# Performance work log

Measured on AMD Instinct MI355X. Metric: run time of the kernel, lower is better.

## Reference

```python
import jax, jax.numpy as jnp
import numpy as np
from jax import lax

B, W, RSS, NLED, LED_F, HID = 8192, 512, 12, 16, 8, 64


def setup_inputs() -> dict:
    key = jax.random.key(0)
    ks = jax.random.split(key, 20)
    s = 0.05
    return {
        "rss_chunk": jax.random.normal(ks[0], (B, W, RSS), jnp.float32),
        "anchor_pos": jax.random.normal(ks[1], (B, 3), jnp.float32),
        "led_feats": jax.random.normal(ks[2], (NLED, LED_F), jnp.float32),
        "led_positions": jax.random.normal(ks[3], (NLED, 3), jnp.float32),
        "freq_mask": jax.random.randint(ks[4], (RSS, NLED), 0, 2, jnp.int32),
        # temporal_conv params (torch Conv1d weight layout [out, in, k])
        "conv1_w": jax.random.normal(ks[5], (32, RSS, 3), jnp.float32) * s,
        "conv1_b": jax.random.normal(ks[6], (32,), jnp.float32) * s,
        "conv2_w": jax.random.normal(ks[7], (64, 32, 3), jnp.float32) * s,
        "conv2_b": jax.random.normal(ks[8], (64,), jnp.float32) * s,
        # projections (torch Linear weight layout [out, in])
        "q_w": jax.random.normal(ks[9], (64, W + 3), jnp.float32) * s,
        "q_b": jax.random.normal(ks[10], (64,), jnp.float32) * s,
        "k_w": jax.random.normal(ks[11], (64, LED_F + 3), jnp.float32) * s,
        "k_b": jax.random.normal(ks[12], (64,), jnp.float32) * s,
        "red_w": jax.random.normal(ks[13], (64, RSS * LED_F), jnp.float32) * s,
        "red_b": jax.random.normal(ks[14], (64,), jnp.float32) * s,
        "fus_w": jax.random.normal(ks[15], (HID, 64 + 64), jnp.float32) * s,
        "fus_b": jax.random.normal(ks[16], (HID,), jnp.float32) * s,
    }


def _conv1d(x, w, b, stride):
    # x: [B, C_in, L], w: [C_out, C_in, k], padding 1
    y = lax.conv_general_dilated(x, w, (stride,), [(1, 1)],
                                 dimension_numbers=("NCH", "OIH", "NCH"))
    return y + b[None, :, None]


def reference(rss_chunk, anchor_pos, led_feats, led_positions, freq_mask,
              conv1_w, conv1_b, conv2_w, conv2_b,
              q_w, q_b, k_w, k_b, red_w, red_b, fus_w, fus_b):
    Bc = rss_chunk.shape[0]
    x = jnp.swapaxes(rss_chunk, 1, 2)                       # [B, 12, W]

    # temporal conv branch -> [B, 64]
    h = jax.nn.relu(_conv1d(x, conv1_w, conv1_b, 1))        # [B, 32, W]
    h = jax.nn.relu(_conv1d(h, conv2_w, conv2_b, 2))        # [B, 64, W//2]
    t_feat = h.mean(axis=-1)                                # AdaptiveAvgPool1d(1)

    # queries: [B, 12, W+3] -> [B, 12, 64]
    pos_rep = jnp.broadcast_to(anchor_pos[:, None, :], (Bc, RSS, 3))
    query_in = jnp.concatenate([x, pos_rep], axis=-1)
    queries = query_in @ q_w.T + q_b

    # keys: [N, 11] -> [N, 64] (shared across batch)
    key_in = jnp.concatenate([led_feats, led_positions], axis=-1)
    keys = key_in @ k_w.T + k_b

    scores = jnp.einsum("brd,nd->brn", queries, keys)       # [B, 12, N]
    dist_sq = jnp.sum((anchor_pos[:, None, :] - led_positions[None, :, :]) ** 2, -1)
    dist_bias = 0.5 * jnp.log(1.0 / (dist_sq + 1e-8))       # [B, N]
    scores = scores + dist_bias[:, None, :]
    scores = jnp.where(freq_mask[None] == 0, jnp.finfo(scores.dtype).min, scores)

    attn = jax.nn.softmax(scores, axis=-1)                  # [B, 12, N]
    s_agg = jnp.einsum("brn,nf->brf", attn, led_feats)      # [B, 12, 8]
    s_feat = jax.nn.relu(s_agg.reshape(Bc, -1) @ red_w.T + red_b)  # [B, 64]

    combined = jnp.concatenate([t_feat, s_feat], axis=-1)   # [B, 128]
    return combined @ fus_w.T + fus_b                       # [B, hidden]
```

## Files before the change

kernel.cpp:

```cpp
#include <hip/hip_runtime.h>
#include <float.h>
#include <math.h>

typedef __bf16 bf16;
typedef __attribute__((ext_vector_type(8))) __bf16 bf16x8;
typedef __attribute__((ext_vector_type(4))) float f32x4;
typedef long long i64;

#define MK 544

#define WS_MG   0
#define WS_CVEC 17408
#define WS_W1F  17472
#define WS_W2F  19520

__device__ __forceinline__ f32x4 mfma16(bf16x8 a, bf16x8 b, f32x4 c) {
  return __builtin_amdgcn_mfma_f32_16x16x32_bf16(a, b, c, 0, 0, 0);
}
__device__ __forceinline__ f32x4 mfma8(i64 a, i64 b, f32x4 c) {
  return __builtin_amdgcn_mfma_f32_16x16x32_fp8_fp8(a, b, c, 0, 0, 0);
}

__global__ __launch_bounds__(256) void acek_pre(
    const float* __restrict__ led_feats, const float* __restrict__ led_pos,
    const float* __restrict__ q_w, const float* __restrict__ q_b,
    const float* __restrict__ k_w, const float* __restrict__ k_b,
    const float* __restrict__ c1w, const float* __restrict__ c2w,
    char* __restrict__ ws) {
  bf16* Mg = (bf16*)(ws + WS_MG);
  float* cvec = (float*)(ws + WS_CVEC);
  i64* W1F = (i64*)(ws + WS_W1F);
  i64* W2F = (i64*)(ws + WS_W2F);
  const int t = threadIdx.x;

  if (blockIdx.x == 34) {
    {
      int ot = t >> 7, s = (t >> 6) & 1, lane = t & 63;
      int g = lane >> 4, a15 = lane & 15;
      float v[8];
#pragma unroll
      for (int j = 0; j < 8; ++j) {
        int k1 = s * 32 + g * 8 + j;
        int dk = k1 >> 4, ic = k1 & 15;
        v[j] = (ic < 12 && dk < 3) ? 16.f * c1w[(ot * 16 + a15) * 36 + ic * 3 + dk] : 0.f;
      }
      int lo = __builtin_amdgcn_cvt_pk_fp8_f32(v[0], v[1], 0, false);
      lo = __builtin_amdgcn_cvt_pk_fp8_f32(v[2], v[3], lo, true);
      int hi = __builtin_amdgcn_cvt_pk_fp8_f32(v[4], v[5], 0, false);
      hi = __builtin_amdgcn_cvt_pk_fp8_f32(v[6], v[7], hi, true);
      W1F[t] = ((i64)(unsigned)lo) | (((i64)hi) << 32);
    }
    for (int r = 0; r < 3; ++r) {
      int fi = t + r * 256;
      int o = fi / 192, rem = fi - o * 192;
      int s = rem >> 6, lane = rem & 63;
      int g = lane >> 4, a15 = lane & 15;
      float v[8];
#pragma unroll
      for (int j = 0; j < 8; ++j)
        v[j] = 16.f * c2w[(o * 16 + a15) * 96 + (g * 8 + j) * 3 + s];
      int lo = __builtin_amdgcn_cvt_pk_fp8_f32(v[0], v[1], 0, false);
      lo = __builtin_amdgcn_cvt_pk_fp8_f32(v[2], v[3], lo, true);
      int hi = __builtin_amdgcn_cvt_pk_fp8_f32(v[4], v[5], 0, false);
      hi = __builtin_amdgcn_cvt_pk_fp8_f32(v[6], v[7], hi, true);
      W2F[fi] = ((i64)(unsigned)lo) | (((i64)hi) << 32);
    }
    return;
  }

  __shared__ float keys[16 * 64];
  for (int idx = t; idx < 16 * 64; idx += 256) {
    int n = idx >> 6, d = idx & 63;
    float acc = k_b[d];
#pragma unroll
    for (int j = 0; j < 8; ++j) acc += k_w[d * 11 + j] * led_feats[n * 8 + j];
#pragma unroll
    for (int j = 0; j < 3; ++j) acc += k_w[d * 11 + 8 + j] * led_pos[n * 3 + j];
    keys[idx] = acc;
  }
  __syncthreads();
  int e = blockIdx.x * 256 + t;
  if (e < 16 * MK) {
    int n = e / MK, k = e - n * MK;
    float v = 0.f;
    if (k < 515) {
#pragma unroll 4
      for (int d = 0; d < 64; ++d) v += q_w[d * 515 + k] * keys[n * 64 + d];
    }
    Mg[e] = (bf16)v;
  }
  if (blockIdx.x == 0 && t < 16) {
    float acc = 0.f;
    for (int d = 0; d < 64; ++d) acc += q_b[d] * keys[t * 64 + d];
    cvec[t] = acc;
  }
}

__global__ __launch_bounds__(256, 4) void acek_main(
    const float* __restrict__ rss, const float* __restrict__ anchor,
    const float* __restrict__ ledf, const float* __restrict__ ledp,
    const int* __restrict__ fmask,
    const float* __restrict__ c1b, const float* __restrict__ c2b,
    const float* __restrict__ rw, const float* __restrict__ rb,
    const float* __restrict__ fw, const float* __restrict__ fb,
    const bf16* __restrict__ Mg, const float* __restrict__ cvec,
    const i64* __restrict__ W1F, const i64* __restrict__ W2F,
    float* __restrict__ out) {

  __shared__ __align__(16) unsigned char xw8[515 * 16];
  __shared__ __align__(16) unsigned char h1[513 * 32];
  __shared__ __align__(16) float parts[1024];
  __shared__ __align__(16) float sagg[96];
  __shared__ __align__(16) float bias_lds[16];
  __shared__ __align__(16) float tfp[256];
  __shared__ __align__(16) float comb[128];

  const int tid = threadIdx.x;
  const int lane = tid & 63;
  const int wv = tid >> 6;
  const int a15 = lane & 15;
  const int g = lane >> 4;
  const int b = blockIdx.x;
  char* xwb = (char*)xw8;
  char* h1b = (char*)h1;

  i64 w1f[2][2];
#pragma unroll
  for (int ot = 0; ot < 2; ++ot)
#pragma unroll
    for (int s = 0; s < 2; ++s) w1f[ot][s] = W1F[(ot * 2 + s) * 64 + lane];
  i64 w2f[4][3];
#pragma unroll
  for (int o = 0; o < 4; ++o)
#pragma unroll
    for (int s = 0; s < 3; ++s) w2f[o][s] = W2F[(o * 3 + s) * 64 + lane];
  f32x4 b1v[2], b2s[4];
#pragma unroll
  for (int ot = 0; ot < 2; ++ot) b1v[ot] = *(const f32x4*)&c1b[ot * 16 + g * 4];
#pragma unroll
  for (int o = 0; o < 4; ++o) {
    f32x4 tmp = *(const f32x4*)&c2b[o * 16 + g * 4];
    b2s[o] = tmp * 16.f;
  }

  if (wv == 0 && lane < 4) *(int*)(xwb + lane * 4) = 0;
  if (wv == 3 && lane < 8)
    *(int*)(xwb + (513 + (lane >> 2)) * 16 + (lane & 3) * 4) = 0;
  if (wv == 0 && lane >= 4 && lane < 8)
    *(i64*)(h1b + (lane - 4) * 8) = 0;
#pragma unroll
  for (int i = 0; i < 3; ++i) {
    int k = lane + 64 * i;
    int r = wv * 128 - 1 + k;
    if (k < 132 && r >= 0 && r <= 514) *(int*)(xwb + r * 16 + 12) = 0;
  }
  if (tid < 16) {
    float dx = anchor[(size_t)b * 3 + 0] - ledp[tid * 3 + 0];
    float dy = anchor[(size_t)b * 3 + 1] - ledp[tid * 3 + 1];
    float dz = anchor[(size_t)b * 3 + 2] - ledp[tid * 3 + 2];
    bias_lds[tid] = cvec[tid] - 0.5f * __logf(dx * dx + dy * dy + dz * dz + 1e-8f);
  }

  const float* xb = rss + (size_t)b * 6144;
  const f32x4* xb4 = (const f32x4*)xb;
  auto stage_px = [&](int w, int hc, f32x4 v) {
    int pk = __builtin_amdgcn_cvt_pk_fp8_f32(16.f * v[0], 16.f * v[1], 0, false);
    pk = __builtin_amdgcn_cvt_pk_fp8_f32(16.f * v[2], 16.f * v[3], pk, true);
    *(int*)(xwb + (w + 1) * 16 + hc * 4) = pk;
  };
#pragma unroll
  for (int i = 0; i < 6; ++i) {
    int f = wv * 384 + lane + 64 * i;
    int w = f / 3;
    int c = f - w * 3;
    stage_px(w, c, xb4[f]);
  }
  if (wv > 0 && lane < 6) {
    int hw = wv * 128 - 2 + lane / 3;
    int hc = lane - (lane / 3) * 3;
    stage_px(hw, hc, xb4[hw * 3 + hc]);
  }
  if (wv < 3 && lane >= 6 && lane < 12) {
    int l2 = lane - 6;
    int hw = wv * 128 + 128 + l2 / 3;
    int hc = l2 - (l2 / 3) * 3;
    stage_px(hw, hc, xb4[hw * 3 + hc]);
  }

  auto conv1_tile = [&](int wt, bool edgeOnly) {
    const int wcol = wt * 16 + a15;
    f32x4 c0 = {0.f, 0.f, 0.f, 0.f}, c1 = {0.f, 0.f, 0.f, 0.f};
#pragma unroll
    for (int s = 0; s < 2; ++s) {
      int row = wcol + 2 * s + (g >> 1);
      i64 bv = *(const i64*)(xwb + row * 16 + ((g & 1) << 3));
      c0 = mfma8(w1f[0][s], bv, c0);
      c1 = mfma8(w1f[1][s], bv, c1);
    }
    if (edgeOnly && a15 != 15) return;
    const int hrow = wcol + 1;
    const int swz = (hrow >> 2) & 3;
    const int off0 = ((((g >> 1) + 0) ^ swz) << 3) | ((g & 1) << 2);
    const int off1 = ((((g >> 1) + 2) ^ swz) << 3) | ((g & 1) << 2);
    float v0 = fmaxf(fmaf(c0[0], 0.00390625f, b1v[0][0]), 0.f);
    float v1 = fmaxf(fmaf(c0[1], 0.00390625f, b1v[0][1]), 0.f);
    float v2 = fmaxf(fmaf(c0[2], 0.00390625f, b1v[0][2]), 0.f);
    float v3 = fmaxf(fmaf(c0[3], 0.00390625f, b1v[0][3]), 0.f);
    int pk0 = __builtin_amdgcn_cvt_pk_fp8_f32(v0, v1, 0, false);
    pk0 = __builtin_amdgcn_cvt_pk_fp8_f32(v2, v3, pk0, true);
    *(int*)(h1b + hrow * 32 + off0) = pk0;
    v0 = fmaxf(fmaf(c1[0], 0.00390625f, b1v[1][0]), 0.f);
    v1 = fmaxf(fmaf(c1[1], 0.00390625f, b1v[1][1]), 0.f);
    v2 = fmaxf(fmaf(c1[2], 0.00390625f, b1v[1][2]), 0.f);
    v3 = fmaxf(fmaf(c1[3], 0.00390625f, b1v[1][3]), 0.f);
    int pk1 = __builtin_amdgcn_cvt_pk_fp8_f32(v0, v1, 0, false);
    pk1 = __builtin_amdgcn_cvt_pk_fp8_f32(v2, v3, pk1, true);
    *(int*)(h1b + hrow * 32 + off1) = pk1;
  };
#pragma unroll
  for (int t = 0; t < 8; ++t) conv1_tile(wv * 8 + t, false);
  if (wv > 0) conv1_tile(wv * 8 - 1, true);

  {
    const int rcl = (a15 < 12) ? a15 : 11;
    float sav[4][8];
#pragma unroll
    for (int t = 0; t < 4; ++t) {
      const int s = 4 * t + wv;
      const float* xs = xb + (s * 32 + g * 8) * 12 + rcl;
#pragma unroll
      for (int j = 0; j < 8; ++j) sav[t][j] = xs[j * 12];
    }
    const bf16* MgR = Mg + a15 * MK;
    f32x4 sac = {0.f, 0.f, 0.f, 0.f};
#pragma unroll
    for (int t = 0; t < 4; ++t) {
      const int s = 4 * t + wv;
      bf16x8 av;
#pragma unroll
      for (int j = 0; j < 8; ++j) av[j] = (bf16)sav[t][j];
      bf16x8 bm = *(const bf16x8*)&MgR[s * 32 + g * 8];
      sac = mfma16(av, bm, sac);
    }
    if (wv == 0) {
      bf16x8 av = {(bf16)0.f, (bf16)0.f, (bf16)0.f, (bf16)0.f,
                   (bf16)0.f, (bf16)0.f, (bf16)0.f, (bf16)0.f};
      if (g == 0) {
        av[0] = (bf16)anchor[(size_t)b * 3 + 0];
        av[1] = (bf16)anchor[(size_t)b * 3 + 1];
        av[2] = (bf16)anchor[(size_t)b * 3 + 2];
      }
      bf16x8 bm = *(const bf16x8*)&MgR[512 + g * 8];
      sac = mfma16(av, bm, sac);
    }
#pragma unroll
    for (int r = 0; r < 4; ++r)
      parts[wv * 256 + (g * 4 + r) * 16 + a15] = sac[r];
  }

  {
    float tacc[4][4] = {{0.f, 0.f, 0.f, 0.f}, {0.f, 0.f, 0.f, 0.f},
                        {0.f, 0.f, 0.f, 0.f}, {0.f, 0.f, 0.f, 0.f}};
#pragma unroll
    for (int pti = 0; pti < 4; ++pti) {
      const int p = (wv * 4 + pti) * 16 + a15;
      f32x4 cc0 = {0.f, 0.f, 0.f, 0.f}, cc1 = {0.f, 0.f, 0.f, 0.f};
      f32x4 cc2 = {0.f, 0.f, 0.f, 0.f}, cc3 = {0.f, 0.f, 0.f, 0.f};
#pragma unroll
      for (int s = 0; s < 3; ++s) {
        const int rho = 2 * p + s;
        i64 hv = *(const i64*)(h1b + rho * 32 + ((g ^ ((rho >> 2) & 3)) << 3));
        cc0 = mfma8(w2f[0][s], hv, cc0);
        cc1 = mfma8(w2f[1][s], hv, cc1);
        cc2 = mfma8(w2f[2][s], hv, cc2);
        cc3 = mfma8(w2f[3][s], hv, cc3);
      }
#pragma unroll
      for (int r = 0; r < 4; ++r) {
        tacc[0][r] += fmaxf(cc0[r] + b2s[0][r], 0.f);
        tacc[1][r] += fmaxf(cc1[r] + b2s[1][r], 0.f);
        tacc[2][r] += fmaxf(cc2[r] + b2s[2][r], 0.f);
        tacc[3][r] += fmaxf(cc3[r] + b2s[3][r], 0.f);
      }
    }
#pragma unroll
    for (int o = 0; o < 4; ++o)
#pragma unroll
      for (int r = 0; r < 4; ++r) {
        float v = tacc[o][r];
        v += __shfl_xor(v, 1, 16);
        v += __shfl_xor(v, 2, 16);
        v += __shfl_xor(v, 4, 16);
        v += __shfl_xor(v, 8, 16);
        if (a15 == 0) tfp[wv * 64 + o * 16 + g * 4 + r] = v;
      }
  }
  __syncthreads();

  if (wv == 0) {
    const int n = a15;
#pragma unroll
    for (int it = 0; it < 3; ++it) {
      const int r = g + 4 * it;
      float s = parts[r * 16 + n] + parts[256 + r * 16 + n] +
                parts[512 + r * 16 + n] + parts[768 + r * 16 + n];
      s += bias_lds[n];
      if (fmask[r * 16 + n] == 0) s = -FLT_MAX;
      float mx = s;
      mx = fmaxf(mx, __shfl_xor(mx, 1, 16));
      mx = fmaxf(mx, __shfl_xor(mx, 2, 16));
      mx = fmaxf(mx, __shfl_xor(mx, 4, 16));
      mx = fmaxf(mx, __shfl_xor(mx, 8, 16));
      float ev = __expf(s - mx);
      float sm = ev;
      sm += __shfl_xor(sm, 1, 16);
      sm += __shfl_xor(sm, 2, 16);
      sm += __shfl_xor(sm, 4, 16);
      sm += __shfl_xor(sm, 8, 16);
      const float attv = ev / sm;
#pragma unroll
      for (int f = 0; f < 8; ++f) {
        float c = attv * ledf[n * 8 + f];
        c += __shfl_xor(c, 1, 16);
        c += __shfl_xor(c, 2, 16);
        c += __shfl_xor(c, 4, 16);
        c += __shfl_xor(c, 8, 16);
        if (n == f) sagg[r * 8 + f] = c;
      }
    }
    comb[lane] = (tfp[lane] + tfp[64 + lane] + tfp[128 + lane] + tfp[192 + lane]) *
                 (1.f / 4096.f);
    {
      float acc = rb[lane];
      const f32x4* rwv = (const f32x4*)(rw + lane * 96);
#pragma unroll
      for (int i = 0; i < 24; ++i) {
        f32x4 a = rwv[i];
        f32x4 sv = *(const f32x4*)&sagg[i * 4];
        acc += a[0] * sv[0] + a[1] * sv[1] + a[2] * sv[2] + a[3] * sv[3];
      }
      comb[64 + lane] = fmaxf(acc, 0.f);
    }
    {
      float acc = fb[lane];
      const f32x4* fwv = (const f32x4*)(fw + lane * 128);
#pragma unroll
      for (int i = 0; i < 32; ++i) {
        f32x4 a = fwv[i];
        f32x4 c = *(const f32x4*)&comb[i * 4];
        acc += a[0] * c[0] + a[1] * c[1] + a[2] * c[2] + a[3] * c[3];
      }
      out[(size_t)b * 64 + lane] = acc;
    }
  }
}

extern "C" void kernel_launch(void* const* d_in, const int* in_sizes, int n_in,
                              void* d_out, int out_size, void* d_ws, size_t ws_size,
                              hipStream_t stream) {
  (void)in_sizes; (void)n_in; (void)out_size; (void)ws_size;
  const float* rss   = (const float*)d_in[0];
  const float* anch  = (const float*)d_in[1];
  const float* ledf  = (const float*)d_in[2];
  const float* ledp  = (const float*)d_in[3];
  const int*   fmask = (const int*)d_in[4];
  const float* c1w = (const float*)d_in[5];
  const float* c1b = (const float*)d_in[6];
  const float* c2w = (const float*)d_in[7];
  const float* c2b = (const float*)d_in[8];
  const float* qw  = (const float*)d_in[9];
  const float* qb  = (const float*)d_in[10];
  const float* kw  = (const float*)d_in[11];
  const float* kb  = (const float*)d_in[12];
  const float* rw  = (const float*)d_in[13];
  const float* rb  = (const float*)d_in[14];
  const float* fw  = (const float*)d_in[15];
  const float* fb  = (const float*)d_in[16];
  float* outp = (float*)d_out;
  char* ws = (char*)d_ws;

  acek_pre<<<35, 256, 0, stream>>>(ledf, ledp, qw, qb, kw, kb, c1w, c2w, ws);
  acek_main<<<8192, 256, 0, stream>>>(
      rss, anch, ledf, ledp, fmask, c1b, c2b, rw, rb, fw, fb,
      (const bf16*)(ws + WS_MG), (const float*)(ws + WS_CVEC),
      (const i64*)(ws + WS_W1F), (const i64*)(ws + WS_W2F), outp);
}
```

Measured before the change: 150.9 us.

## Process one batch element per wavefront with a ring-buffered conv1 output

Instead of a 256-thread block cooperating on one batch row, each wavefront now handles a whole batch element on its own, with the grid reduced to 2048 blocks of four. The conv1 output is kept in a small 48-row ring buffer that conv2 consumes tile by tile, so the full per-element conv1 buffer is no longer stored. This removes the block-wide __syncthreads and the cross-wave reduction through LDS, and cuts shared memory per element. In exchange each wave does serial work across the whole sequence with less intra-element parallelism, and its strided global reads for the query projection may have worse coalescing.

Result: faster. 130.0 us (-13.8%).

```diff
diff --git a/kernel.cpp b/kernel.cpp
--- a/kernel.cpp
+++ b/kernel.cpp
@@ -107,22 +107,19 @@
     const i64* __restrict__ W1F, const i64* __restrict__ W2F,
     float* __restrict__ out) {
 
-  __shared__ __align__(16) unsigned char xw8[515 * 16];
-  __shared__ __align__(16) unsigned char h1[513 * 32];
-  __shared__ __align__(16) float parts[1024];
-  __shared__ __align__(16) float sagg[96];
-  __shared__ __align__(16) float bias_lds[16];
-  __shared__ __align__(16) float tfp[256];
-  __shared__ __align__(16) float comb[128];
+  __shared__ __align__(16) unsigned char pool[4][9792];
 
   const int tid = threadIdx.x;
   const int lane = tid & 63;
   const int wv = tid >> 6;
   const int a15 = lane & 15;
   const int g = lane >> 4;
-  const int b = blockIdx.x;
-  char* xwb = (char*)xw8;
-  char* h1b = (char*)h1;
+  const int b = blockIdx.x * 4 + wv;
+
+  char* xw = (char*)pool[wv];
+  char* ring = (char*)pool[wv] + 8240;
+  float* sagg = (float*)pool[wv];
+  float* comb = (float*)(pool[wv] + 8240);
 
   i64 w1f[2][2];
 #pragma unroll
@@ -143,133 +140,76 @@
     b2s[o] = tmp * 16.f;
   }
 
-  if (wv == 0 && lane < 4) *(int*)(xwb + lane * 4) = 0;
-  if (wv == 3 && lane < 8)
-    *(int*)(xwb + (513 + (lane >> 2)) * 16 + (lane & 3) * 4) = 0;
-  if (wv == 0 && lane >= 4 && lane < 8)
-    *(i64*)(h1b + (lane - 4) * 8) = 0;
-#pragma unroll
-  for (int i = 0; i < 3; ++i) {
-    int k = lane + 64 * i;
-    int r = wv * 128 - 1 + k;
-    if (k < 132 && r >= 0 && r <= 514) *(int*)(xwb + r * 16 + 12) = 0;
-  }
-  if (tid < 16) {
-    float dx = anchor[(size_t)b * 3 + 0] - ledp[tid * 3 + 0];
-    float dy = anchor[(size_t)b * 3 + 1] - ledp[tid * 3 + 1];
-    float dz = anchor[(size_t)b * 3 + 2] - ledp[tid * 3 + 2];
-    bias_lds[tid] = cvec[tid] - 0.5f * __logf(dx * dx + dy * dy + dz * dz + 1e-8f);
-  }
+  for (int r = lane; r < 515; r += 64) *(int*)(xw + r * 16 + 12) = 0;
+  if (lane < 12) {
+    int rr = (lane >> 2) == 0 ? 0 : ((lane >> 2) == 1 ? 513 : 514);
+    *(int*)(xw + rr * 16 + (lane & 3) * 4) = 0;
+  }
+  if (lane < 4) *(i64*)(ring + lane * 8) = 0;
 
   const float* xb = rss + (size_t)b * 6144;
   const f32x4* xb4 = (const f32x4*)xb;
-  auto stage_px = [&](int w, int hc, f32x4 v) {
+#pragma unroll
+  for (int i = 0; i < 24; ++i) {
+    int f = lane + 64 * i;
+    f32x4 v = xb4[f];
+    int w = f / 3;
+    int c = f - w * 3;
     int pk = __builtin_amdgcn_cvt_pk_fp8_f32(16.f * v[0], 16.f * v[1], 0, false);
     pk = __builtin_amdgcn_cvt_pk_fp8_f32(16.f * v[2], 16.f * v[3], pk, true);
-    *(int*)(xwb + (w + 1) * 16 + hc * 4) = pk;
-  };
-#pragma unroll
-  for (int i = 0; i < 6; ++i) {
-    int f = wv * 384 + lane + 64 * i;
-    int w = f / 3;
-    int c = f - w * 3;
-    stage_px(w, c, xb4[f]);
-  }
-  if (wv > 0 && lane < 6) {
-    int hw = wv * 128 - 2 + lane / 3;
-    int hc = lane - (lane / 3) * 3;
-    stage_px(hw, hc, xb4[hw * 3 + hc]);
-  }
-  if (wv < 3 && lane >= 6 && lane < 12) {
-    int l2 = lane - 6;
-    int hw = wv * 128 + 128 + l2 / 3;
-    int hc = l2 - (l2 / 3) * 3;
-    stage_px(hw, hc, xb4[hw * 3 + hc]);
-  }
-
-  auto conv1_tile = [&](int wt, bool edgeOnly) {
-    const int wcol = wt * 16 + a15;
-    f32x4 c0 = {0.f, 0.f, 0.f, 0.f}, c1 = {0.f, 0.f, 0.f, 0.f};
-#pragma unroll
-    for (int s = 0; s < 2; ++s) {
-      int row = wcol + 2 * s + (g >> 1);
-      i64 bv = *(const i64*)(xwb + row * 16 + ((g & 1) << 3));
-      c0 = mfma8(w1f[0][s], bv, c0);
-      c1 = mfma8(w1f[1][s], bv, c1);
-    }
-    if (edgeOnly && a15 != 15) return;
-    const int hrow = wcol + 1;
-    const int swz = (hrow >> 2) & 3;
-    const int off0 = ((((g >> 1) + 0) ^ swz) << 3) | ((g & 1) << 2);
-    const int off1 = ((((g >> 1) + 2) ^ swz) << 3) | ((g & 1) << 2);
-    float v0 = fmaxf(fmaf(c0[0], 0.00390625f, b1v[0][0]), 0.f);
-    float v1 = fmaxf(fmaf(c0[1], 0.00390625f, b1v[0][1]), 0.f);
-    float v2 = fmaxf(fmaf(c0[2], 0.00390625f, b1v[0][2]), 0.f);
-    float v3 = fmaxf(fmaf(c0[3], 0.00390625f, b1v[0][3]), 0.f);
-    int pk0 = __builtin_amdgcn_cvt_pk_fp8_f32(v0, v1, 0, false);
-    pk0 = __builtin_amdgcn_cvt_pk_fp8_f32(v2, v3, pk0, true);
-    *(int*)(h1b + hrow * 32 + off0) = pk0;
-    v0 = fmaxf(fmaf(c1[0], 0.00390625f, b1v[1][0]), 0.f);
-    v1 = fmaxf(fmaf(c1[1], 0.00390625f, b1v[1][1]), 0.f);
-    v2 = fmaxf(fmaf(c1[2], 0.00390625f, b1v[1][2]), 0.f);
-    v3 = fmaxf(fmaf(c1[3], 0.00390625f, b1v[1][3]), 0.f);
-    int pk1 = __builtin_amdgcn_cvt_pk_fp8_f32(v0, v1, 0, false);
-    pk1 = __builtin_amdgcn_cvt_pk_fp8_f32(v2, v3, pk1, true);
-    *(int*)(h1b + hrow * 32 + off1) = pk1;
-  };
-#pragma unroll
-  for (int t = 0; t < 8; ++t) conv1_tile(wv * 8 + t, false);
-  if (wv > 0) conv1_tile(wv * 8 - 1, true);
-
-  {
-    const int rcl = (a15 < 12) ? a15 : 11;
-    float sav[4][8];
-#pragma unroll
-    for (int t = 0; t < 4; ++t) {
-      const int s = 4 * t + wv;
-      const float* xs = xb + (s * 32 + g * 8) * 12 + rcl;
-#pragma unroll
-      for (int j = 0; j < 8; ++j) sav[t][j] = xs[j * 12];
-    }
-    const bf16* MgR = Mg + a15 * MK;
-    f32x4 sac = {0.f, 0.f, 0.f, 0.f};
-#pragma unroll
-    for (int t = 0; t < 4; ++t) {
-      const int s = 4 * t + wv;
-      bf16x8 av;
-#pragma unroll
-      for (int j = 0; j < 8; ++j) av[j] = (bf16)sav[t][j];
-      bf16x8 bm = *(const bf16x8*)&MgR[s * 32 + g * 8];
-      sac = mfma16(av, bm, sac);
-    }
-    if (wv == 0) {
-      bf16x8 av = {(bf16)0.f, (bf16)0.f, (bf16)0.f, (bf16)0.f,
-                   (bf16)0.f, (bf16)0.f, (bf16)0.f, (bf16)0.f};
-      if (g == 0) {
-        av[0] = (bf16)anchor[(size_t)b * 3 + 0];
-        av[1] = (bf16)anchor[(size_t)b * 3 + 1];
-        av[2] = (bf16)anchor[(size_t)b * 3 + 2];
+    *(int*)(xw + (w + 1) * 16 + c * 4) = pk;
+  }
+
+  const int icb = (g & 1) << 3;
+  const int dk0 = g >> 1;
+  const int dW[2] = {a15 + 1, a15 + 17};
+  const int dR0 = 2 * a15;
+
+  float tacc[4][4] = {{0.f, 0.f, 0.f, 0.f}, {0.f, 0.f, 0.f, 0.f},
+                      {0.f, 0.f, 0.f, 0.f}, {0.f, 0.f, 0.f, 0.f}};
+  int base = 0;
+  for (int pt = 0; pt < 16; ++pt) {
+#pragma unroll
+    for (int e = 0; e < 2; ++e) {
+      f32x4 c0 = {0.f, 0.f, 0.f, 0.f}, c1 = {0.f, 0.f, 0.f, 0.f};
+#pragma unroll
+      for (int s = 0; s < 2; ++s) {
+        int row = 32 * pt + 16 * e + a15 + 2 * s + dk0;
+        i64 bv = *(const i64*)(xw + row * 16 + icb);
+        c0 = mfma8(w1f[0][s], bv, c0);
+        c1 = mfma8(w1f[1][s], bv, c1);
       }
-      bf16x8 bm = *(const bf16x8*)&MgR[512 + g * 8];
-      sac = mfma16(av, bm, sac);
-    }
-#pragma unroll
-    for (int r = 0; r < 4; ++r)
-      parts[wv * 256 + (g * 4 + r) * 16 + a15] = sac[r];
-  }
-
-  {
-    float tacc[4][4] = {{0.f, 0.f, 0.f, 0.f}, {0.f, 0.f, 0.f, 0.f},
-                        {0.f, 0.f, 0.f, 0.f}, {0.f, 0.f, 0.f, 0.f}};
-#pragma unroll
-    for (int pti = 0; pti < 4; ++pti) {
-      const int p = (wv * 4 + pti) * 16 + a15;
+      int d = dW[e];
+      int slot = base + d;
+      if (slot >= 48) slot -= 48;
+      int swz = (d >> 2) & 3;
+      int off0 = ((((g >> 1) + 0) ^ swz) << 3) | ((g & 1) << 2);
+      int off1 = ((((g >> 1) + 2) ^ swz) << 3) | ((g & 1) << 2);
+      float v0 = fmaxf(fmaf(c0[0], 0.00390625f, b1v[0][0]), 0.f);
+      float v1 = fmaxf(fmaf(c0[1], 0.00390625f, b1v[0][1]), 0.f);
+      float v2 = fmaxf(fmaf(c0[2], 0.00390625f, b1v[0][2]), 0.f);
+      float v3 = fmaxf(fmaf(c0[3], 0.00390625f, b1v[0][3]), 0.f);
+      int pk0 = __builtin_amdgcn_cvt_pk_fp8_f32(v0, v1, 0, false);
+      pk0 = __builtin_amdgcn_cvt_pk_fp8_f32(v2, v3, pk0, true);
+      *(int*)(ring + slot * 32 + off0) = pk0;
+      v0 = fmaxf(fmaf(c1[0], 0.00390625f, b1v[1][0]), 0.f);
+      v1 = fmaxf(fmaf(c1[1], 0.00390625f, b1v[1][1]), 0.f);
+      v2 = fmaxf(fmaf(c1[2], 0.00390625f, b1v[1][2]), 0.f);
+      v3 = fmaxf(fmaf(c1[3], 0.00390625f, b1v[1][3]), 0.f);
+      int pk1 = __builtin_amdgcn_cvt_pk_fp8_f32(v0, v1, 0, false);
+      pk1 = __builtin_amdgcn_cvt_pk_fp8_f32(v2, v3, pk1, true);
+      *(int*)(ring + slot * 32 + off1) = pk1;
+    }
+    {
       f32x4 cc0 = {0.f, 0.f, 0.f, 0.f}, cc1 = {0.f, 0.f, 0.f, 0.f};
       f32x4 cc2 = {0.f, 0.f, 0.f, 0.f}, cc3 = {0.f, 0.f, 0.f, 0.f};
 #pragma unroll
       for (int s = 0; s < 3; ++s) {
-        const int rho = 2 * p + s;
-        i64 hv = *(const i64*)(h1b + rho * 32 + ((g ^ ((rho >> 2) & 3)) << 3));
+        int d = dR0 + s;
+        int slot = base + d;
+        if (slot >= 48) slot -= 48;
+        int swz = (d >> 2) & 3;
+        i64 hv = *(const i64*)(ring + slot * 32 + ((g ^ swz) << 3));
         cc0 = mfma8(w2f[0][s], hv, cc0);
         cc1 = mfma8(w2f[1][s], hv, cc1);
         cc2 = mfma8(w2f[2][s], hv, cc2);
@@ -283,75 +223,103 @@
         tacc[3][r] += fmaxf(cc3[r] + b2s[3][r], 0.f);
       }
     }
-#pragma unroll
-    for (int o = 0; o < 4; ++o)
-#pragma unroll
-      for (int r = 0; r < 4; ++r) {
-        float v = tacc[o][r];
-        v += __shfl_xor(v, 1, 16);
-        v += __shfl_xor(v, 2, 16);
-        v += __shfl_xor(v, 4, 16);
-        v += __shfl_xor(v, 8, 16);
-        if (a15 == 0) tfp[wv * 64 + o * 16 + g * 4 + r] = v;
-      }
-  }
-  __syncthreads();
-
-  if (wv == 0) {
-    const int n = a15;
-#pragma unroll
-    for (int it = 0; it < 3; ++it) {
-      const int r = g + 4 * it;
-      float s = parts[r * 16 + n] + parts[256 + r * 16 + n] +
-                parts[512 + r * 16 + n] + parts[768 + r * 16 + n];
-      s += bias_lds[n];
-      if (fmask[r * 16 + n] == 0) s = -FLT_MAX;
-      float mx = s;
-      mx = fmaxf(mx, __shfl_xor(mx, 1, 16));
-      mx = fmaxf(mx, __shfl_xor(mx, 2, 16));
-      mx = fmaxf(mx, __shfl_xor(mx, 4, 16));
-      mx = fmaxf(mx, __shfl_xor(mx, 8, 16));
-      float ev = __expf(s - mx);
-      float sm = ev;
-      sm += __shfl_xor(sm, 1, 16);
-      sm += __shfl_xor(sm, 2, 16);
-      sm += __shfl_xor(sm, 4, 16);
-      sm += __shfl_xor(sm, 8, 16);
-      const float attv = ev / sm;
-#pragma unroll
-      for (int f = 0; f < 8; ++f) {
-        float c = attv * ledf[n * 8 + f];
-        c += __shfl_xor(c, 1, 16);
-        c += __shfl_xor(c, 2, 16);
-        c += __shfl_xor(c, 4, 16);
-        c += __shfl_xor(c, 8, 16);
-        if (n == f) sagg[r * 8 + f] = c;
-      }
-    }
-    comb[lane] = (tfp[lane] + tfp[64 + lane] + tfp[128 + lane] + tfp[192 + lane]) *
-                 (1.f / 4096.f);
-    {
-      float acc = rb[lane];
-      const f32x4* rwv = (const f32x4*)(rw + lane * 96);
-#pragma unroll
-      for (int i = 0; i < 24; ++i) {
-        f32x4 a = rwv[i];
-        f32x4 sv = *(const f32x4*)&sagg[i * 4];
-        acc += a[0] * sv[0] + a[1] * sv[1] + a[2] * sv[2] + a[3] * sv[3];
-      }
-      comb[64 + lane] = fmaxf(acc, 0.f);
-    }
-    {
-      float acc = fb[lane];
-      const f32x4* fwv = (const f32x4*)(fw + lane * 128);
-#pragma unroll
-      for (int i = 0; i < 32; ++i) {
-        f32x4 a = fwv[i];
-        f32x4 c = *(const f32x4*)&comb[i * 4];
-        acc += a[0] * c[0] + a[1] * c[1] + a[2] * c[2] + a[3] * c[3];
-      }
-      out[(size_t)b * 64 + lane] = acc;
-    }
+    base += 32;
+    if (base >= 48) base -= 48;
+  }
+
+#pragma unroll
+  for (int o = 0; o < 4; ++o)
+#pragma unroll
+    for (int r = 0; r < 4; ++r) {
+      float v = tacc[o][r];
+      v += __shfl_xor(v, 1, 16);
+      v += __shfl_xor(v, 2, 16);
+      v += __shfl_xor(v, 4, 16);
+      v += __shfl_xor(v, 8, 16);
+      if (a15 == 0) comb[o * 16 + g * 4 + r] = v * (1.f / 4096.f);
+    }
+
+  const int rcl = (a15 < 12) ? a15 : 11;
+  const bf16* MgR = Mg + a15 * MK;
+  f32x4 sac = {0.f, 0.f, 0.f, 0.f};
+#pragma unroll 4
+  for (int s = 0; s < 16; ++s) {
+    const float* xs = xb + (s * 32 + g * 8) * 12 + rcl;
+    bf16x8 av;
+#pragma unroll
+    for (int j = 0; j < 8; ++j) av[j] = (bf16)xs[j * 12];
+    bf16x8 bm = *(const bf16x8*)&MgR[s * 32 + g * 8];
+    sac = mfma16(av, bm, sac);
+  }
+  {
+    bf16x8 av = {(bf16)0.f, (bf16)0.f, (bf16)0.f, (bf16)0.f,
+                 (bf16)0.f, (bf16)0.f, (bf16)0.f, (bf16)0.f};
+    if (g == 0) {
+      av[0] = (bf16)anchor[(size_t)b * 3 + 0];
+      av[1] = (bf16)anchor[(size_t)b * 3 + 1];
+      av[2] = (bf16)anchor[(size_t)b * 3 + 2];
+    }
+    bf16x8 bm = *(const bf16x8*)&MgR[512 + g * 8];
+    sac = mfma16(av, bm, sac);
+  }
+
+  float dx = anchor[(size_t)b * 3 + 0] - ledp[a15 * 3 + 0];
+  float dy = anchor[(size_t)b * 3 + 1] - ledp[a15 * 3 + 1];
+  float dz = anchor[(size_t)b * 3 + 2] - ledp[a15 * 3 + 2];
+  float cv = cvec[a15] - 0.5f * __logf(dx * dx + dy * dy + dz * dz + 1e-8f);
+  const f32x4* lfp = (const f32x4*)(ledf + a15 * 8);
+  f32x4 lfA = lfp[0], lfB = lfp[1];
+#pragma unroll
+  for (int rho = 0; rho < 4; ++rho) {
+    int r = 4 * g + rho;
+    int mrow = (r < 12) ? r : 11;
+    float s = sac[rho] + cv;
+    if (r >= 12 || fmask[mrow * 16 + a15] == 0) s = -FLT_MAX;
+    float mx = s;
+    mx = fmaxf(mx, __shfl_xor(mx, 1, 16));
+    mx = fmaxf(mx, __shfl_xor(mx, 2, 16));
+    mx = fmaxf(mx, __shfl_xor(mx, 4, 16));
+    mx = fmaxf(mx, __shfl_xor(mx, 8, 16));
+    float ev = __expf(s - mx);
+    float sm = ev;
+    sm += __shfl_xor(sm, 1, 16);
+    sm += __shfl_xor(sm, 2, 16);
+    sm += __shfl_xor(sm, 4, 16);
+    sm += __shfl_xor(sm, 8, 16);
+    const float attv = ev / sm;
+#pragma unroll
+    for (int f = 0; f < 8; ++f) {
+      float c = attv * ((f < 4) ? lfA[f] : lfB[f - 4]);
+      c += __shfl_xor(c, 1, 16);
+      c += __shfl_xor(c, 2, 16);
+      c += __shfl_xor(c, 4, 16);
+      c += __shfl_xor(c, 8, 16);
+      if (a15 == f && r < 12) sagg[r * 8 + f] = c;
+    }
+  }
+
+  {
+    float acc = rb[lane];
+    const f32x4* rwv = (const f32x4*)(rw + lane * 96);
+#pragma unroll
+    for (int i = 0; i < 24; ++i) {
+      f32x4 a = rwv[i];
+      f32x4 sv = *(const f32x4*)&sagg[i * 4];
+      acc += a[0] * sv[0] + a[1] * sv[1] + a[2] * sv[2] + a[3] * sv[3];
+    }
+    comb[64 + lane] = fmaxf(acc, 0.f);
+  }
+
+  {
+    float acc = fb[lane];
+    const f32x4* fwv = (const f32x4*)(fw + lane * 128);
+#pragma unroll
+    for (int i = 0; i < 32; ++i) {
+      f32x4 a = fwv[i];
+      f32x4 c = *(const f32x4*)&comb[i * 4];
+      acc += a[0] * c[0] + a[1] * c[1] + a[2] * c[2] + a[3] * c[3];
+    }
+    out[(size_t)b * 64 + lane] = acc;
   }
 }
 
@@ -380,7 +348,7 @@
   char* ws = (char*)d_ws;
 
   acek_pre<<<35, 256, 0, stream>>>(ledf, ledp, qw, qb, kw, kb, c1w, c2w, ws);
-  acek_main<<<8192, 256, 0, stream>>>(
+  acek_main<<<2048, 256, 0, stream>>>(
       rss, anch, ledf, ledp, fmask, c1b, c2b, rw, rb, fw, fb,
       (const bf16*)(ws + WS_MG), (const float*)(ws + WS_CVEC),
       (const i64*)(ws + WS_W1F), (const i64*)(ws + WS_W2F), outp);
```
